# Optimization experiments

Measured on AMD Instinct MI355X. Metric: run time of the kernel, lower is better.

Reference implementation:

```python
import jax, jax.numpy as jnp
import numpy as np

N_NODES = 50000
N_EDGES = 800000
F_IN = 128
HEADS = 2
F_OUT = 128  # out_channels == nfeat for the residual


def setup_inputs() -> dict:
    key = jax.random.key(0)
    k_x, k_e, k_u, k_c, k_w, k_b = jax.random.split(key, 6)
    x = jax.random.normal(k_x, (N_NODES, F_IN), dtype=jnp.float32)
    edge_index = jax.random.randint(k_e, (2, N_EDGES), 0, N_NODES, dtype=jnp.int64)
    # FeaStConv params (PyG init: normal(mean=0, std=0.1))
    u = 0.1 * jax.random.normal(k_u, (F_IN, HEADS), dtype=jnp.float32)       # attention proj
    c = 0.1 * jax.random.normal(k_c, (HEADS,), dtype=jnp.float32)            # attention bias
    w = 0.1 * jax.random.normal(k_w, (F_IN, HEADS * F_OUT), dtype=jnp.float32)  # lin weight
    bias = 0.1 * jax.random.normal(k_b, (F_OUT,), dtype=jnp.float32)
    return {"x": x, "edge_index": edge_index, "u": u, "c": c, "w": w, "bias": bias}


def _feast_conv(x, edge_index, u, c, w, bias):
    n = x.shape[0]
    # add self loops (PyG FeaStConv default add_self_loops=True)
    loops = jnp.arange(n, dtype=edge_index.dtype)
    src = jnp.concatenate([edge_index[0], loops])  # j (source / message sender)
    dst = jnp.concatenate([edge_index[1], loops])  # i (target / aggregator)
    e = src.shape[0]
    # per-edge attention over heads: q = softmax(u^T (x_j - x_i) + c)
    xi = x[dst]                                   # [E, F_in]
    xj = x[src]                                   # [E, F_in]
    q = jax.nn.softmax((xj - xi) @ u + c, axis=-1)  # [E, H]
    # per-node linear, then gather per edge
    xw = (x @ w).reshape(n, HEADS, F_OUT)         # [N, H, F_out]
    msg = jnp.einsum('eh,ehf->ef', q, xw[src])    # [E, F_out]
    # mean aggregation at destinations
    agg = jax.ops.segment_sum(msg, dst, num_segments=n)
    cnt = jax.ops.segment_sum(jnp.ones((e,), x.dtype), dst, num_segments=n)
    return agg / jnp.maximum(cnt, 1.0)[:, None] + bias


def reference(x, edge_index, u, c, w, bias):
    # module forward: x + relu(FeaStConv(x, edge_index))
    return x + jax.nn.relu(_feast_conv(x, edge_index, u, c, w, bias))
```

## Files before the change

### kernel.cpp

```cpp
#include <hip/hip_runtime.h>
#include <hip/hip_bf16.h>

constexpr int N_NODES = 50000;
constexpr int N_EDGES = 800000;
constexpr int F_IN    = 128;
constexpr int F_OUT   = 128;
constexpr int HEADS   = 2;
constexpr int WCOLS   = HEADS * F_OUT;
constexpr int WE_ROWS = 272;
constexpr int SEG     = 64;

typedef __attribute__((ext_vector_type(8))) short  bf16x8;
typedef __attribute__((ext_vector_type(4))) float  f32x4;
typedef __attribute__((ext_vector_type(2))) float  f32x2;

static __device__ __forceinline__ unsigned short f32_to_bf16_bits(float f) {
    unsigned int u = __float_as_uint(f);
    u += 0x7fffu + ((u >> 16) & 1u);
    return (unsigned short)(u >> 16);
}

__global__ __launch_bounds__(256) void wt_cnt_kernel(const float* __restrict__ w,
                                                     const float* __restrict__ u,
                                                     unsigned short* __restrict__ wTe,
                                                     int* __restrict__ cnt) {
    const int tid = blockIdx.x * 256 + threadIdx.x;
    if (tid < WE_ROWS * F_IN) {
        const int r = tid >> 7;
        const int k = tid & 127;
        float v;
        if (r < WCOLS)            v = w[k * WCOLS + r];
        else if (r < WCOLS + 2)   v = u[k * HEADS + (r - WCOLS)];
        else                      v = 0.f;
        wTe[tid] = f32_to_bf16_bits(v);
    }
    if (tid < N_NODES) cnt[tid] = 0;
}

constexpr int RG = 2;

__global__ __launch_bounds__(256) void proj_kernel(const float* __restrict__ x,
                                                   const unsigned short* __restrict__ wTe,
                                                   unsigned char* __restrict__ xwf,
                                                   float2* __restrict__ s_tab) {
    const int lane = threadIdx.x & 63;
    const int wv   = threadIdx.x >> 6;
    const int n0   = blockIdx.x * (16 * RG);
    const int l15  = lane & 15;
    const int kg   = lane >> 4;

    f32x4 acc[RG][4];
    f32x4 acc4[RG];
#pragma unroll
    for (int rg = 0; rg < RG; ++rg) {
        acc4[rg] = (f32x4){0.f, 0.f, 0.f, 0.f};
#pragma unroll
        for (int t = 0; t < 4; ++t) acc[rg][t] = acc4[rg];
    }

#pragma unroll
    for (int ks = 0; ks < 4; ++ks) {
        bf16x8 xf[RG];
#pragma unroll
        for (int rg = 0; rg < RG; ++rg) {
            const int row = min(n0 + rg * 16 + l15, N_NODES - 1);
            const float* xp = x + (size_t)row * F_IN + ks * 32 + kg * 8;
            const float4 xa = *(const float4*)xp;
            const float4 xb = *(const float4*)(xp + 4);
            xf[rg][0] = (short)f32_to_bf16_bits(xa.x);
            xf[rg][1] = (short)f32_to_bf16_bits(xa.y);
            xf[rg][2] = (short)f32_to_bf16_bits(xa.z);
            xf[rg][3] = (short)f32_to_bf16_bits(xa.w);
            xf[rg][4] = (short)f32_to_bf16_bits(xb.x);
            xf[rg][5] = (short)f32_to_bf16_bits(xb.y);
            xf[rg][6] = (short)f32_to_bf16_bits(xb.z);
            xf[rg][7] = (short)f32_to_bf16_bits(xb.w);
        }

        const unsigned short* wbase = wTe + (size_t)(wv * 64 + l15) * F_IN + ks * 32 + kg * 8;
        const bf16x8 wf0 = *(const bf16x8*)(wbase);
        const bf16x8 wf1 = *(const bf16x8*)(wbase + 16 * F_IN);
        const bf16x8 wf2 = *(const bf16x8*)(wbase + 32 * F_IN);
        const bf16x8 wf3 = *(const bf16x8*)(wbase + 48 * F_IN);

#pragma unroll
        for (int rg = 0; rg < RG; ++rg) {
            acc[rg][0] = __builtin_amdgcn_mfma_f32_16x16x32_bf16(wf0, xf[rg], acc[rg][0], 0, 0, 0);
            acc[rg][1] = __builtin_amdgcn_mfma_f32_16x16x32_bf16(wf1, xf[rg], acc[rg][1], 0, 0, 0);
            acc[rg][2] = __builtin_amdgcn_mfma_f32_16x16x32_bf16(wf2, xf[rg], acc[rg][2], 0, 0, 0);
            acc[rg][3] = __builtin_amdgcn_mfma_f32_16x16x32_bf16(wf3, xf[rg], acc[rg][3], 0, 0, 0);
        }
        if (wv == 3) {
            const unsigned short* ubase = wTe + (size_t)(256 + l15) * F_IN + ks * 32 + kg * 8;
            const bf16x8 uf = *(const bf16x8*)(ubase);
#pragma unroll
            for (int rg = 0; rg < RG; ++rg)
                acc4[rg] = __builtin_amdgcn_mfma_f32_16x16x32_bf16(uf, xf[rg], acc4[rg], 0, 0, 0);
        }
    }

#pragma unroll
    for (int rg = 0; rg < RG; ++rg) {
        const int row = n0 + rg * 16 + l15;
        if (row < N_NODES) {
            unsigned char* orow = xwf + (size_t)row * WCOLS + wv * 64 + kg * 4;
#pragma unroll
            for (int t = 0; t < 4; ++t) {
                unsigned int pk = 0;
                pk = __builtin_amdgcn_cvt_pk_fp8_f32(acc[rg][t][0], acc[rg][t][1], pk, false);
                pk = __builtin_amdgcn_cvt_pk_fp8_f32(acc[rg][t][2], acc[rg][t][3], pk, true);
                *(unsigned int*)(orow + t * 16) = pk;
            }
            if (wv == 3 && kg == 0) {
                s_tab[row] = make_float2(acc4[rg][0], acc4[rg][1]);
            }
        }
    }
}

constexpr int EPB = 4;

__global__ __launch_bounds__(256) void scatter_kernel(const int* __restrict__ ei,
                                                      const float2* __restrict__ s,
                                                      const float* __restrict__ c,
                                                      int* __restrict__ cnt,
                                                      unsigned int* __restrict__ rec) {
    const int base = blockIdx.x * (256 * EPB) + threadIdx.x;
    const float c0 = c[0], c1 = c[1];

    int  srcv[EPB], dstv[EPB], pos[EPB];
    bool val[EPB];
#pragma unroll
    for (int k = 0; k < EPB; ++k) {
        const int e  = base + k * 256;
        val[k] = (e < N_EDGES);
        const int ec = val[k] ? e : 0;
        srcv[k] = ei[ec];
        dstv[k] = ei[N_EDGES + ec];
    }
#pragma unroll
    for (int k = 0; k < EPB; ++k) {
        pos[k] = val[k] ? atomicAdd(&cnt[dstv[k]], 1) : 0;
    }
    float qv[EPB];
#pragma unroll
    for (int k = 0; k < EPB; ++k) {
        const float2 ss = s[srcv[k]];
        const float2 sd = s[dstv[k]];
        const float l0 = ss.x - sd.x + c0;
        const float l1 = ss.y - sd.y + c1;
        const float m  = fmaxf(l0, l1);
        const float e0 = __expf(l0 - m);
        const float e1 = __expf(l1 - m);
        qv[k] = e0 / (e0 + e1);
    }
#pragma unroll
    for (int k = 0; k < EPB; ++k) {
        if (val[k]) {
            const unsigned int q16 = (unsigned int)(qv[k] * 65535.0f + 0.5f);
            const int p = min(pos[k], SEG - 1);
            rec[(size_t)dstv[k] * SEG + p] = (q16 << 16) | (unsigned int)srcv[k];
        }
    }
}

#define AGG_SLOT(K, A)                                                        \
    {                                                                         \
        const unsigned int r = rp[j + K];                                     \
        const unsigned int g = *(const unsigned int*)(gb + (size_t)(r & 0xffffu) * WCOLS); \
        const float q = fmaf(qsign, (float)(r >> 16) * (1.0f/65535.0f), qbase);\
        const f32x2 glo = __builtin_amdgcn_cvt_pk_f32_fp8(g, false);          \
        const f32x2 ghi = __builtin_amdgcn_cvt_pk_f32_fp8(g, true);           \
        A.x = fmaf(q, glo[0], A.x);                                           \
        A.y = fmaf(q, glo[1], A.y);                                           \
        A.z = fmaf(q, ghi[0], A.z);                                           \
        A.w = fmaf(q, ghi[1], A.w);                                           \
    }

__global__ __launch_bounds__(256) void agg_kernel(const float* __restrict__ x,
                                                  const float* __restrict__ bias,
                                                  const float* __restrict__ c,
                                                  const unsigned char* __restrict__ xwf,
                                                  const unsigned int* __restrict__ rec,
                                                  const int* __restrict__ cnt,
                                                  float* __restrict__ out) {
    const int lane = threadIdx.x & 63;
    const int half = lane >> 5;
    const int l5   = lane & 31;
    const int n    = blockIdx.x * 4 + (threadIdx.x >> 6);
    if (n >= N_NODES) return;
    const int m_cnt = min(cnt[n], SEG);
    const int deg   = m_cnt + 1;
    const unsigned int* rp = rec + (size_t)n * SEG;

    const float qbase = half ? 1.0f : 0.0f;
    const float qsign = half ? -1.0f : 1.0f;
    const unsigned char* gb = xwf + half * F_OUT + 4 * l5;

    const float c0 = c[0], c1 = c[1];
    const float mm = fmaxf(c0, c1);
    const float se0 = __expf(c0 - mm);
    const float se1 = __expf(c1 - mm);
    const float qs = fmaf(qsign, se0 / (se0 + se1), qbase);
    const unsigned int gsv = *(const unsigned int*)(gb + (size_t)n * WCOLS);
    const f32x2 slo = __builtin_amdgcn_cvt_pk_f32_fp8(gsv, false);
    const f32x2 shi = __builtin_amdgcn_cvt_pk_f32_fp8(gsv, true);
    float4 a0, a1 = {0.f,0.f,0.f,0.f}, a2 = a1, a3 = a1;
    a0.x = qs * slo[0];
    a0.y = qs * slo[1];
    a0.z = qs * shi[0];
    a0.w = qs * shi[1];

    int j = 0;
    for (; j + 4 <= m_cnt; j += 4) {
        AGG_SLOT(0, a0) AGG_SLOT(1, a1) AGG_SLOT(2, a2) AGG_SLOT(3, a3)
    }
    for (; j < m_cnt; ++j) {
        AGG_SLOT(0, a0)
    }
    float4 t;
    t.x = (a0.x + a1.x) + (a2.x + a3.x);
    t.y = (a0.y + a1.y) + (a2.y + a3.y);
    t.z = (a0.z + a1.z) + (a2.z + a3.z);
    t.w = (a0.w + a1.w) + (a2.w + a3.w);
    t.x += __shfl_xor(t.x, 32, 64);
    t.y += __shfl_xor(t.y, 32, 64);
    t.z += __shfl_xor(t.z, 32, 64);
    t.w += __shfl_xor(t.w, 32, 64);
    if (half == 0) {
        const float inv = 1.0f / (float)deg;
        const float4 bv = *(const float4*)(bias + 4 * l5);
        const float4 xv = *(const float4*)(x + (size_t)n * F_IN + 4 * l5);
        float4 r;
        r.x = xv.x + fmaxf(fmaf(t.x, inv, bv.x), 0.f);
        r.y = xv.y + fmaxf(fmaf(t.y, inv, bv.y), 0.f);
        r.z = xv.z + fmaxf(fmaf(t.z, inv, bv.z), 0.f);
        r.w = xv.w + fmaxf(fmaf(t.w, inv, bv.w), 0.f);
        *(float4*)(out + (size_t)n * F_OUT + 4 * l5) = r;
    }
}

extern "C" void kernel_launch(void* const* d_in, const int* in_sizes, int n_in,
                              void* d_out, int out_size, void* d_ws, size_t ws_size,
                              hipStream_t stream) {
    const float* x    = (const float*)d_in[0];
    const int*   ei   = (const int*)  d_in[1];
    const float* u    = (const float*)d_in[2];
    const float* c    = (const float*)d_in[3];
    const float* w    = (const float*)d_in[4];
    const float* bias = (const float*)d_in[5];
    float* out = (float*)d_out;

    char* p = (char*)d_ws;
    unsigned char* xwf = (unsigned char*)p;    p += (size_t)N_NODES * WCOLS;
    float2* s_tab  = (float2*)p;               p += (size_t)N_NODES * sizeof(float2);
    int*    cnt    = (int*)p;                  p += (size_t)N_NODES * sizeof(int);
    unsigned short* wTe = (unsigned short*)p;  p += (size_t)WE_ROWS * F_IN * sizeof(unsigned short);
    unsigned int* rec = (unsigned int*)p;

    wt_cnt_kernel<<<(N_NODES + 255) / 256, 256, 0, stream>>>(w, u, wTe, cnt);

    proj_kernel<<<(N_NODES + 16 * RG - 1) / (16 * RG), 256, 0, stream>>>(x, wTe, xwf, s_tab);

    scatter_kernel<<<(N_EDGES + 256 * EPB - 1) / (256 * EPB), 256, 0, stream>>>(ei, s_tab, c, cnt, rec);

    agg_kernel<<<(N_NODES + 3) / 4, 256, 0, stream>>>(x, bias, c, xwf, rec, cnt, out);
}
```

Before: 132.0 us.

## Partition edge scatter by destination range and enlarge projection row groups

The scatter kernel now launches 8 blocks per edge chunk, each handling only edges whose destination falls in one eighth of the node range. The goal is to localize the atomic counter updates and record writes so they hit the cache better. The cost is that every block reads the destination indices 8 times, and the grid is 8x larger with mostly idle lanes. Separately, the projection kernel processes 4 row groups per block instead of 2, which raises per-block reuse of the weights at the cost of more registers.

```diff
diff --git a/kernel.cpp b/kernel.cpp
--- a/kernel.cpp
+++ b/kernel.cpp
@@ -37,7 +37,7 @@
     if (tid < N_NODES) cnt[tid] = 0;
 }
 
-constexpr int RG = 2;
+constexpr int RG = 4;
 
 __global__ __launch_bounds__(256) void proj_kernel(const float* __restrict__ x,
                                                    const unsigned short* __restrict__ wTe,
@@ -118,46 +118,52 @@
     }
 }
 
-constexpr int EPB = 4;
+constexpr int EPT    = 4;
+constexpr int CHUNK  = 256 * EPT;
+constexpr int NCHUNK = (N_EDGES + CHUNK - 1) / CHUNK;
+constexpr int NGROUP = 8;
+constexpr int DRANGE = N_NODES / NGROUP;
 
 __global__ __launch_bounds__(256) void scatter_kernel(const int* __restrict__ ei,
                                                       const float2* __restrict__ s,
                                                       const float* __restrict__ c,
                                                       int* __restrict__ cnt,
                                                       unsigned int* __restrict__ rec) {
-    const int base = blockIdx.x * (256 * EPB) + threadIdx.x;
+    const int g     = blockIdx.x & (NGROUP - 1);
+    const int chunk = blockIdx.x >> 3;
+    const int dlo   = g * DRANGE;
+    const int dhi   = dlo + DRANGE;
+    const int base  = chunk * CHUNK + threadIdx.x;
     const float c0 = c[0], c1 = c[1];
 
-    int  srcv[EPB], dstv[EPB], pos[EPB];
-    bool val[EPB];
-#pragma unroll
-    for (int k = 0; k < EPB; ++k) {
-        const int e  = base + k * 256;
-        val[k] = (e < N_EDGES);
-        const int ec = val[k] ? e : 0;
-        srcv[k] = ei[ec];
+    int  dstv[EPT];
+    bool keep[EPT];
+#pragma unroll
+    for (int k = 0; k < EPT; ++k) {
+        const int e = base + k * 256;
+        const int ec = (e < N_EDGES) ? e : 0;
         dstv[k] = ei[N_EDGES + ec];
-    }
-#pragma unroll
-    for (int k = 0; k < EPB; ++k) {
-        pos[k] = val[k] ? atomicAdd(&cnt[dstv[k]], 1) : 0;
-    }
-    float qv[EPB];
-#pragma unroll
-    for (int k = 0; k < EPB; ++k) {
-        const float2 ss = s[srcv[k]];
-        const float2 sd = s[dstv[k]];
-        const float l0 = ss.x - sd.x + c0;
-        const float l1 = ss.y - sd.y + c1;
-        const float m  = fmaxf(l0, l1);
-        const float e0 = __expf(l0 - m);
-        const float e1 = __expf(l1 - m);
-        qv[k] = e0 / (e0 + e1);
-    }
-#pragma unroll
-    for (int k = 0; k < EPB; ++k) {
-        if (val[k]) {
-            const unsigned int q16 = (unsigned int)(qv[k] * 65535.0f + 0.5f);
+        keep[k] = (e < N_EDGES) && (dstv[k] >= dlo) && (dstv[k] < dhi);
+    }
+    int pos[EPT], srcv[EPT];
+#pragma unroll
+    for (int k = 0; k < EPT; ++k) {
+        pos[k]  = keep[k] ? atomicAdd(&cnt[dstv[k]], 1) : 0;
+        const int e = base + k * 256;
+        srcv[k] = keep[k] ? ei[e] : 0;
+    }
+#pragma unroll
+    for (int k = 0; k < EPT; ++k) {
+        if (keep[k]) {
+            const float2 ss = s[srcv[k]];
+            const float2 sd = s[dstv[k]];
+            const float l0 = ss.x - sd.x + c0;
+            const float l1 = ss.y - sd.y + c1;
+            const float m  = fmaxf(l0, l1);
+            const float e0 = __expf(l0 - m);
+            const float e1 = __expf(l1 - m);
+            const float q0 = e0 / (e0 + e1);
+            const unsigned int q16 = (unsigned int)(q0 * 65535.0f + 0.5f);
             const int p = min(pos[k], SEG - 1);
             rec[(size_t)dstv[k] * SEG + p] = (q16 << 16) | (unsigned int)srcv[k];
         }
@@ -262,7 +268,7 @@
 
     proj_kernel<<<(N_NODES + 16 * RG - 1) / (16 * RG), 256, 0, stream>>>(x, wTe, xwf, s_tab);
 
-    scatter_kernel<<<(N_EDGES + 256 * EPB - 1) / (256 * EPB), 256, 0, stream>>>(ei, s_tab, c, cnt, rec);
+    scatter_kernel<<<NGROUP * NCHUNK, 256, 0, stream>>>(ei, s_tab, c, cnt, rec);
 
     agg_kernel<<<(N_NODES + 3) / 4, 256, 0, stream>>>(x, bias, c, xwf, rec, cnt, out);
 }
```

Result: faster. 123.6 us (-6.4%).
